# Kernel tuning notes

Hardware: AMD Instinct MI355X
Metric: run time of the kernel (lower is better)

Reference implementation:

```python
import jax, jax.numpy as jnp
import numpy as np
from jax import lax

B, CIN, COUT, H, W, K = 32, 256, 256, 56, 56, 3

def setup_inputs() -> dict:
    key = jax.random.key(0)
    k1, k2, k3 = jax.random.split(key, 3)
    inp = jax.random.normal(k1, (B, CIN, H, W), dtype=jnp.float32)
    # kaiming-style init for conv kernel, normal init for bias
    fan_in = CIN * K * K
    kernel = jax.random.normal(k2, (COUT, CIN, K, K), dtype=jnp.float32) * np.float32(np.sqrt(2.0 / fan_in))
    bias = jax.random.normal(k3, (COUT,), dtype=jnp.float32)
    return {"inp": inp, "kernel": kernel, "bias": bias}

def reference(inp, kernel, bias):
    # Equivalent to the crossbar path: im2col 3x3 patches @ stacked [kernel|bias]
    # matrix == standard conv2d(padding=1, stride=1) + bias.
    out = lax.conv_general_dilated(
        inp, kernel,
        window_strides=(1, 1),
        padding=((1, 1), (1, 1)),
        dimension_numbers=("NCHW", "OIHW", "NCHW"),
    )
    return out + bias[None, :, None, None]
```

## Files before the change

### kernel.cpp

```cpp
#include <hip/hip_runtime.h>
#include <hip/hip_bf16.h>


#define BB    32
#define CINC  256
#define COUTC 256
#define HH    56
#define WW    56
#define HP    58
#define WP    58
#define PIX_PER_IMG 3136
#define NPIX  100352
#define KTOT  2304
#define NKT   72

#define XT_BYTES ((size_t)BB*HP*WP*CINC*2)
#define WR_ELEMS ((size_t)COUTC*KTOT)
#define WR_BYTES (WR_ELEMS*2)

#define BUF_SZ 24576
#define B_OFF  16384

using frag_t = __attribute__((ext_vector_type(8))) short;
using f32x4  = __attribute__((ext_vector_type(4))) float;

__device__ __forceinline__ void gload_lds16(const void* gsrc, void* ldst) {
  __builtin_amdgcn_global_load_lds(
      (const __attribute__((address_space(1))) unsigned*)gsrc,
      (__attribute__((address_space(3))) unsigned*)ldst, 16, 0, 0);
}

__global__ void xpose_kernel(const float* __restrict__ inp,
                             __hip_bfloat16* __restrict__ xt) {
  int bid = blockIdx.x;
  int hp = bid % HP;
  int t  = bid / HP;
  int cb = t % 4;
  int b  = t / 4;
  __shared__ __hip_bfloat16 tile[64 * 60];
  int tid = threadIdx.x;
  for (int i = tid; i < 64 * 60; i += 256) tile[i] = __float2bfloat16(0.f);
  __syncthreads();
  int h = hp - 1;
  if (h >= 0 && h < HH) {
    const float* src = inp + ((size_t)(b * CINC + cb * 64) * HH + h) * WW;
    for (int i = tid; i < 64 * WW; i += 256) {
      int ci = i / WW, w = i - ci * WW;
      tile[ci * 60 + (w + 1)] = __float2bfloat16(src[(size_t)ci * HH * WW + w]);
    }
  }
  __syncthreads();
  __hip_bfloat16* dst = xt + ((size_t)(b * HP + hp) * WP) * CINC + cb * 64;
  for (int i = tid; i < WP * 64; i += 256) {
    int wp = i >> 6, ci = i & 63;
    dst[(size_t)wp * CINC + ci] = tile[ci * 60 + wp];
  }
}

__global__ void wprep_kernel(const float* __restrict__ k4,
                             __hip_bfloat16* __restrict__ wr) {
  int i = blockIdx.x * 256 + threadIdx.x;
  if (i >= (int)WR_ELEMS) return;
  int co = i / KTOT;
  int k  = i - co * KTOT;
  int tap = k >> 8;
  int ci  = k & 255;
  wr[i] = __float2bfloat16(k4[(co * CINC + ci) * 9 + tap]);
}

__global__ __launch_bounds__(256, 2) void conv_p16(
    const __hip_bfloat16* __restrict__ xt,
    const __hip_bfloat16* __restrict__ wr,
    const float* __restrict__ bias,
    float* __restrict__ out) {
  __shared__ alignas(16) char lds[3 * BUF_SZ];

  const int tid  = threadIdx.x;
  const int lane = tid & 63;
  const int wid  = tid >> 6;
  const int wm   = wid >> 1;
  const int wn   = wid & 1;
  const int fr   = lane & 15;
  const int g    = lane >> 4;

  const int bid   = blockIdx.x;
  const int ntile = (bid & 7) * 98 + (bid >> 3);

  const char* wr_b = (const char*)wr;
  const char* xt_b = (const char*)xt;

  const int lr  = lane >> 2;
  const int sc  = ((((lane & 3) - ((lane >> 3) & 3)) & 3) << 4);

  const char* pA0 = wr_b + (size_t)(wid * 64 +  0 + lr) * (KTOT * 2) + sc;
  const char* pA1 = wr_b + (size_t)(wid * 64 + 16 + lr) * (KTOT * 2) + sc;
  const char* pA2 = wr_b + (size_t)(wid * 64 + 32 + lr) * (KTOT * 2) + sc;
  const char* pA3 = wr_b + (size_t)(wid * 64 + 48 + lr) * (KTOT * 2) + sc;

  auto mkB = [&](int jb) -> const char* {
    int px = ntile * 128 + wid * 32 + jb * 16 + lr;
    int b  = px / PIX_PER_IMG;
    int hw = px - b * PIX_PER_IMG;
    int h = hw / WW, w = hw - h * WW;
    return xt_b + (size_t)((b * HP + h) * WP + w) * (CINC * 2) + sc;
  };
  const char* pB0 = mkB(0);
  const char* pB1 = mkB(1);

#define STG(T2, WB) {                                                      \
    size_t _ao = (size_t)(T2) * 64;                                        \
    int _tap = (T2) >> 3; int _rr = _tap / 3, _ss = _tap - _rr * 3;        \
    size_t _bo = (size_t)(_rr * WP + _ss) * (CINC * 2)                     \
               + (size_t)((T2) & 7) * 64;                                  \
    char* _d = lds + (WB) * BUF_SZ;                                        \
    gload_lds16(pA0 + _ao, _d + wid * 4096 + 0);                           \
    gload_lds16(pA1 + _ao, _d + wid * 4096 + 1024);                        \
    gload_lds16(pA2 + _ao, _d + wid * 4096 + 2048);                        \
    gload_lds16(pA3 + _ao, _d + wid * 4096 + 3072);                        \
    gload_lds16(pB0 + _bo, _d + B_OFF + wid * 2048 + 0);                   \
    gload_lds16(pB1 + _bo, _d + B_OFF + wid * 2048 + 1024); }

  const int ckr   = (((g + (fr >> 1)) & 3) << 4);
  const int aroff = (wm * 128 + fr) * 64 + ckr;
  const int broff = B_OFF + (wn * 64 + fr) * 64 + ckr;

  frag_t fa[8], fb[4];
  f32x4 acc[8][4] = {};

#define RSL(RB) {                                                          \
    const char* _b = lds + (RB) * BUF_SZ;                                  \
    _Pragma("unroll") for (int m = 0; m < 8; ++m)                          \
      fa[m] = *(const frag_t*)(_b + aroff + m * 1024);                     \
    _Pragma("unroll") for (int n = 0; n < 4; ++n)                          \
      fb[n] = *(const frag_t*)(_b + broff + n * 1024); }

#define MF() {                                                             \
    __builtin_amdgcn_s_setprio(1);                                         \
    _Pragma("unroll") for (int m = 0; m < 8; ++m)                          \
    _Pragma("unroll") for (int n = 0; n < 4; ++n)                          \
      acc[m][n] = __builtin_amdgcn_mfma_f32_16x16x32_bf16(                 \
          fa[m], fb[n], acc[m][n], 0, 0, 0);                               \
    __builtin_amdgcn_s_setprio(0); }

#define BODY(T, RB, WB) {                                                  \
    STG((T) + 2, WB);                                                      \
    RSL(RB);                                                               \
    MF();                                                                  \
    asm volatile("s_waitcnt vmcnt(6)" ::: "memory");                       \
    __builtin_amdgcn_s_barrier();                                          \
    __builtin_amdgcn_sched_barrier(0); }

  STG(0, 0);
  STG(1, 1);
  asm volatile("s_waitcnt vmcnt(6)" ::: "memory");
  __builtin_amdgcn_s_barrier();
  __builtin_amdgcn_sched_barrier(0);

  for (int base = 0; base < 69; base += 3) {
    BODY(base + 0, 0, 2);
    BODY(base + 1, 1, 0);
    BODY(base + 2, 2, 1);
  }
  BODY(69, 0, 2);
  {
    RSL(1);
    MF();
    asm volatile("s_waitcnt vmcnt(0)" ::: "memory");
    __builtin_amdgcn_s_barrier();
    __builtin_amdgcn_sched_barrier(0);
  }
  {
    RSL(2);
    MF();
  }

  int pb[4], phw[4];
#pragma unroll
  for (int n = 0; n < 4; ++n) {
    int pxg = ntile * 128 + wn * 64 + n * 16 + fr;
    pb[n]  = pxg / PIX_PER_IMG;
    phw[n] = pxg - pb[n] * PIX_PER_IMG;
  }
#pragma unroll
  for (int m = 0; m < 8; ++m) {
#pragma unroll
    for (int rg = 0; rg < 4; ++rg) {
      int co = wm * 128 + m * 16 + g * 4 + rg;
      float bv = bias[co];
#pragma unroll
      for (int n = 0; n < 4; ++n)
        out[((size_t)pb[n] * COUTC + co) * PIX_PER_IMG + phw[n]] =
            acc[m][n][rg] + bv;
    }
  }
}

__global__ void conv_direct(const float* __restrict__ inp,
                            const float* __restrict__ kern,
                            const float* __restrict__ bias,
                            float* __restrict__ out) {
  int idx = blockIdx.x * 256 + threadIdx.x;
  if (idx >= BB * COUTC * PIX_PER_IMG) return;
  int w = idx % WW;
  int t = idx / WW;
  int h = t % HH; t /= HH;
  int co = t % COUTC;
  int b  = t / COUTC;
  float acc = bias[co];
  for (int ci = 0; ci < CINC; ++ci)
    for (int r = 0; r < 3; ++r) {
      int hh = h + r - 1;
      if (hh < 0 || hh >= HH) continue;
      for (int s = 0; s < 3; ++s) {
        int ww2 = w + s - 1;
        if (ww2 < 0 || ww2 >= WW) continue;
        acc += inp[((size_t)(b * CINC + ci) * HH + hh) * WW + ww2] *
               kern[(co * CINC + ci) * 9 + r * 3 + s];
      }
    }
  out[idx] = acc;
}

extern "C" void kernel_launch(void* const* d_in, const int* in_sizes, int n_in,
                              void* d_out, int out_size, void* d_ws, size_t ws_size,
                              hipStream_t stream) {
  const float* inp  = (const float*)d_in[0];
  const float* kern = (const float*)d_in[1];
  const float* bias = (const float*)d_in[2];
  float* out = (float*)d_out;

  size_t need = XT_BYTES + WR_BYTES;
  if (ws_size < need) {
    int tot = BB * COUTC * PIX_PER_IMG;
    conv_direct<<<(tot + 255) / 256, 256, 0, stream>>>(inp, kern, bias, out);
    return;
  }

  __hip_bfloat16* xt  = (__hip_bfloat16*)d_ws;
  __hip_bfloat16* wrp = (__hip_bfloat16*)((char*)d_ws + XT_BYTES);

  xpose_kernel<<<BB * 4 * HP, 256, 0, stream>>>(inp, xt);
  wprep_kernel<<<(int)((WR_ELEMS + 255) / 256), 256, 0, stream>>>(kern, wrp);
  conv_p16<<<NPIX / 128, 256, 0, stream>>>(xt, wrp, bias, out);
}
```

Baseline: 186.0 us.

## Pre-pack weights into MFMA fragment order and load A directly into registers

The weight prep kernel now writes bf16 weights already laid out as per-lane MFMA A fragments, so the conv kernel loads them straight from global memory into registers instead of staging them through LDS. The A fragments are double-buffered in registers (fa0/fa1), prefetched one K-step ahead, and only the B (activation) tiles still go through a smaller triple-buffered LDS ring. This removes LDS traffic and LDS footprint for A, but each wave pair now fetches the same weight fragments from global/L2 separately and needs 8 more fragment registers, which can hurt occupancy or add vmem latency.

```diff
diff --git a/kernel.cpp b/kernel.cpp
--- a/kernel.cpp
+++ b/kernel.cpp
@@ -15,11 +15,10 @@
 #define NKT   72
 
 #define XT_BYTES ((size_t)BB*HP*WP*CINC*2)
-#define WR_ELEMS ((size_t)COUTC*KTOT)
-#define WR_BYTES (WR_ELEMS*2)
-
-#define BUF_SZ 24576
-#define B_OFF  16384
+#define AWR_FRAGS (72*16*64)
+#define AWR_BYTES ((size_t)AWR_FRAGS*16)
+
+#define BUF_SZ 8192
 
 using frag_t = __attribute__((ext_vector_type(8))) short;
 using f32x4  = __attribute__((ext_vector_type(4))) float;
@@ -57,20 +56,30 @@
   }
 }
 
-__global__ void wprep_kernel(const float* __restrict__ k4,
-                             __hip_bfloat16* __restrict__ wr) {
+__global__ void wprep_pack(const float* __restrict__ k4,
+                           frag_t* __restrict__ awr) {
   int i = blockIdx.x * 256 + threadIdx.x;
-  if (i >= (int)WR_ELEMS) return;
-  int co = i / KTOT;
-  int k  = i - co * KTOT;
-  int tap = k >> 8;
-  int ci  = k & 255;
-  wr[i] = __float2bfloat16(k4[(co * CINC + ci) * 9 + tap]);
-}
-
-__global__ __launch_bounds__(256, 2) void conv_p16(
+  if (i >= AWR_FRAGS) return;
+  int lane = i & 63;
+  int mb   = (i >> 6) & 15;
+  int t    = i >> 10;
+  int co   = mb * 16 + (lane & 15);
+  int kb   = t * 32 + (lane >> 4) * 8;
+  frag_t v;
+#pragma unroll
+  for (int j = 0; j < 8; ++j) {
+    int k = kb + j;
+    int tap = k >> 8;
+    int ci  = k & 255;
+    __hip_bfloat16 h = __float2bfloat16(k4[(co * CINC + ci) * 9 + tap]);
+    v[j] = *reinterpret_cast<short*>(&h);
+  }
+  awr[i] = v;
+}
+
+__global__ __launch_bounds__(256, 2) void conv_areg(
     const __hip_bfloat16* __restrict__ xt,
-    const __hip_bfloat16* __restrict__ wr,
+    const frag_t* __restrict__ awr,
     const float* __restrict__ bias,
     float* __restrict__ out) {
   __shared__ alignas(16) char lds[3 * BUF_SZ];
@@ -86,16 +95,10 @@
   const int bid   = blockIdx.x;
   const int ntile = (bid & 7) * 98 + (bid >> 3);
 
-  const char* wr_b = (const char*)wr;
   const char* xt_b = (const char*)xt;
 
   const int lr  = lane >> 2;
   const int sc  = ((((lane & 3) - ((lane >> 3) & 3)) & 3) << 4);
-
-  const char* pA0 = wr_b + (size_t)(wid * 64 +  0 + lr) * (KTOT * 2) + sc;
-  const char* pA1 = wr_b + (size_t)(wid * 64 + 16 + lr) * (KTOT * 2) + sc;
-  const char* pA2 = wr_b + (size_t)(wid * 64 + 32 + lr) * (KTOT * 2) + sc;
-  const char* pA3 = wr_b + (size_t)(wid * 64 + 48 + lr) * (KTOT * 2) + sc;
 
   auto mkB = [&](int jb) -> const char* {
     int px = ntile * 128 + wid * 32 + jb * 16 + lr;
@@ -108,70 +111,79 @@
   const char* pB1 = mkB(1);
 
 #define STG(T2, WB) {                                                      \
-    size_t _ao = (size_t)(T2) * 64;                                        \
     int _tap = (T2) >> 3; int _rr = _tap / 3, _ss = _tap - _rr * 3;        \
     size_t _bo = (size_t)(_rr * WP + _ss) * (CINC * 2)                     \
                + (size_t)((T2) & 7) * 64;                                  \
     char* _d = lds + (WB) * BUF_SZ;                                        \
-    gload_lds16(pA0 + _ao, _d + wid * 4096 + 0);                           \
-    gload_lds16(pA1 + _ao, _d + wid * 4096 + 1024);                        \
-    gload_lds16(pA2 + _ao, _d + wid * 4096 + 2048);                        \
-    gload_lds16(pA3 + _ao, _d + wid * 4096 + 3072);                        \
-    gload_lds16(pB0 + _bo, _d + B_OFF + wid * 2048 + 0);                   \
-    gload_lds16(pB1 + _bo, _d + B_OFF + wid * 2048 + 1024); }
+    gload_lds16(pB0 + _bo, _d + wid * 2048 + 0);                           \
+    gload_lds16(pB1 + _bo, _d + wid * 2048 + 1024); }
+
+  const frag_t* abase = awr + (size_t)(wm * 8) * 64 + lane;
+
+#define ALOAD(T1, FA) {                                                    \
+    const frag_t* _p = abase + (size_t)(T1) * (16 * 64);                   \
+    _Pragma("unroll") for (int m = 0; m < 8; ++m)                          \
+      FA[m] = _p[m * 64]; }
 
   const int ckr   = (((g + (fr >> 1)) & 3) << 4);
-  const int aroff = (wm * 128 + fr) * 64 + ckr;
-  const int broff = B_OFF + (wn * 64 + fr) * 64 + ckr;
-
-  frag_t fa[8], fb[4];
+  const int broff = (wn * 64 + fr) * 64 + ckr;
+
+  frag_t fa0[8], fa1[8], fb[4];
   f32x4 acc[8][4] = {};
 
 #define RSL(RB) {                                                          \
     const char* _b = lds + (RB) * BUF_SZ;                                  \
-    _Pragma("unroll") for (int m = 0; m < 8; ++m)                          \
-      fa[m] = *(const frag_t*)(_b + aroff + m * 1024);                     \
     _Pragma("unroll") for (int n = 0; n < 4; ++n)                          \
       fb[n] = *(const frag_t*)(_b + broff + n * 1024); }
 
-#define MF() {                                                             \
+#define MF(FA) {                                                           \
     __builtin_amdgcn_s_setprio(1);                                         \
     _Pragma("unroll") for (int m = 0; m < 8; ++m)                          \
     _Pragma("unroll") for (int n = 0; n < 4; ++n)                          \
       acc[m][n] = __builtin_amdgcn_mfma_f32_16x16x32_bf16(                 \
-          fa[m], fb[n], acc[m][n], 0, 0, 0);                               \
+          FA[m], fb[n], acc[m][n], 0, 0, 0);                               \
     __builtin_amdgcn_s_setprio(0); }
 
-#define BODY(T, RB, WB) {                                                  \
+#define BODY(T, RB, WB, FCUR, FNXT) {                                      \
     STG((T) + 2, WB);                                                      \
+    ALOAD((T) + 1, FNXT);                                                  \
     RSL(RB);                                                               \
-    MF();                                                                  \
-    asm volatile("s_waitcnt vmcnt(6)" ::: "memory");                       \
+    MF(FCUR);                                                              \
+    asm volatile("s_waitcnt vmcnt(10)" ::: "memory");                      \
     __builtin_amdgcn_s_barrier();                                          \
     __builtin_amdgcn_sched_barrier(0); }
 
   STG(0, 0);
   STG(1, 1);
-  asm volatile("s_waitcnt vmcnt(6)" ::: "memory");
+  ALOAD(0, fa0);
+  asm volatile("s_waitcnt vmcnt(10)" ::: "memory");
   __builtin_amdgcn_s_barrier();
   __builtin_amdgcn_sched_barrier(0);
 
-  for (int base = 0; base < 69; base += 3) {
-    BODY(base + 0, 0, 2);
-    BODY(base + 1, 1, 0);
-    BODY(base + 2, 2, 1);
-  }
-  BODY(69, 0, 2);
+  for (int base = 0; base < 66; base += 6) {
+    BODY(base + 0, 0, 2, fa0, fa1);
+    BODY(base + 1, 1, 0, fa1, fa0);
+    BODY(base + 2, 2, 1, fa0, fa1);
+    BODY(base + 3, 0, 2, fa1, fa0);
+    BODY(base + 4, 1, 0, fa0, fa1);
+    BODY(base + 5, 2, 1, fa1, fa0);
+  }
+  BODY(66, 0, 2, fa0, fa1);
+  BODY(67, 1, 0, fa1, fa0);
+  BODY(68, 2, 1, fa0, fa1);
+  BODY(69, 0, 2, fa1, fa0);
+
   {
+    ALOAD(71, fa1);
     RSL(1);
-    MF();
+    MF(fa0);
     asm volatile("s_waitcnt vmcnt(0)" ::: "memory");
     __builtin_amdgcn_s_barrier();
     __builtin_amdgcn_sched_barrier(0);
   }
   {
     RSL(2);
-    MF();
+    MF(fa1);
   }
 
   int pb[4], phw[4];
@@ -229,17 +241,17 @@
   const float* bias = (const float*)d_in[2];
   float* out = (float*)d_out;
 
-  size_t need = XT_BYTES + WR_BYTES;
+  size_t need = XT_BYTES + AWR_BYTES;
   if (ws_size < need) {
     int tot = BB * COUTC * PIX_PER_IMG;
     conv_direct<<<(tot + 255) / 256, 256, 0, stream>>>(inp, kern, bias, out);
     return;
   }
 
-  __hip_bfloat16* xt  = (__hip_bfloat16*)d_ws;
-  __hip_bfloat16* wrp = (__hip_bfloat16*)((char*)d_ws + XT_BYTES);
+  __hip_bfloat16* xt = (__hip_bfloat16*)d_ws;
+  frag_t* awr = (frag_t*)((char*)d_ws + XT_BYTES);
 
   xpose_kernel<<<BB * 4 * HP, 256, 0, stream>>>(inp, xt);
-  wprep_kernel<<<(int)((WR_ELEMS + 255) / 256), 256, 0, stream>>>(kern, wrp);
-  conv_p16<<<NPIX / 128, 256, 0, stream>>>(xt, wrp, bias, out);
-}
+  wprep_pack<<<(AWR_FRAGS + 255) / 256, 256, 0, stream>>>(kern, awr);
+  conv_areg<<<NPIX / 128, 256, 0, stream>>>(xt, awr, bias, out);
+}
```

Result: no change. 185.5 us (-0.2%).
